# Kernel optimization log

Hardware: AMD Instinct MI355X
Metric: run time of the kernel (lower is better)

The kernel has to match this reference:

```python
import jax, jax.numpy as jnp
import numpy as np

N_NODES_PER_GRAPH = 64
NUM_GRAPHS = 2048
N = NUM_GRAPHS * N_NODES_PER_GRAPH  # 131072 total nodes
E = N * 8                           # 1048576 edges
IN_DIM, H1, H2 = 64, 128, 64
OUT_DIM = (N_NODES_PER_GRAPH * N_NODES_PER_GRAPH - N_NODES_PER_GRAPH) // 2  # 2016


def setup_inputs() -> dict:
    key = jax.random.key(0)
    ks = jax.random.split(key, 16)
    s = 0.05
    x = jax.random.normal(ks[0], (N, IN_DIM), dtype=jnp.float32)
    # edges within each graph: offsets within graph + graph base offset
    src_local = jax.random.randint(ks[1], (E,), 0, N_NODES_PER_GRAPH)
    dst_local = jax.random.randint(ks[2], (E,), 0, N_NODES_PER_GRAPH)
    gid = jnp.repeat(jnp.arange(NUM_GRAPHS), E // NUM_GRAPHS) * N_NODES_PER_GRAPH
    edge_index = jnp.stack([src_local + gid, dst_local + gid]).astype(jnp.int64)
    batch = jnp.repeat(jnp.arange(NUM_GRAPHS), N_NODES_PER_GRAPH).astype(jnp.int64)
    eps = jax.random.normal(ks[3], (NUM_GRAPHS, H2), dtype=jnp.float32)
    return {
        "x": x, "edge_index": edge_index, "batch": batch, "eps": eps,
        "w1_rel": jax.random.normal(ks[4], (IN_DIM, H1)) * s,
        "b1": jnp.zeros((H1,), jnp.float32),
        "w1_root": jax.random.normal(ks[5], (IN_DIM, H1)) * s,
        "w2_rel": jax.random.normal(ks[6], (H1, H2)) * s,
        "b2": jnp.zeros((H2,), jnp.float32),
        "w2_root": jax.random.normal(ks[7], (H1, H2)) * s,
        "w3_rel": jax.random.normal(ks[8], (H1, H2)) * s,
        "b3": jnp.zeros((H2,), jnp.float32),
        "w3_root": jax.random.normal(ks[9], (H1, H2)) * s,
        "fc1_w": jax.random.normal(ks[10], (H2, H1)) * s,
        "fc1_b": jnp.zeros((H1,), jnp.float32),
        "fc2_w": jax.random.normal(ks[11], (H1, OUT_DIM)) * s,
        "fc2_b": jnp.zeros((OUT_DIM,), jnp.float32),
    }


def _graph_conv(h, src, dst, w_rel, b, w_root):
    # PyG GraphConv: out_i = W_rel @ (sum_{j in N(i)} h_j) + b + W_root @ h_i
    agg = jax.ops.segment_sum(h[src], dst, num_segments=N)  # [N, d_in]
    return agg @ w_rel + b + h @ w_root


def _segment_mean(h, seg):
    s = jax.ops.segment_sum(h, seg, num_segments=NUM_GRAPHS)
    cnt = jax.ops.segment_sum(jnp.ones((h.shape[0],), h.dtype), seg, num_segments=NUM_GRAPHS)
    return s / jnp.maximum(cnt, 1.0)[:, None]


def reference(x, edge_index, batch, eps, w1_rel, b1, w1_root, w2_rel, b2, w2_root,
              w3_rel, b3, w3_root, fc1_w, fc1_b, fc2_w, fc2_b):
    src, dst = edge_index[0], edge_index[1]
    # encode (dropout p=0.0 -> identity)
    h1 = jax.nn.relu(_graph_conv(x, src, dst, w1_rel, b1, w1_root))
    mu = _segment_mean(_graph_conv(h1, src, dst, w2_rel, b2, w2_root), batch)
    logvar = _segment_mean(_graph_conv(h1, src, dst, w3_rel, b3, w3_root), batch)
    # reparameterize with provided eps
    z = mu + eps * jnp.exp(0.5 * logvar)
    # decode
    h = jax.nn.relu(z @ fc1_w + fc1_b)
    recon = jax.nn.sigmoid(h @ fc2_w + fc2_b)
    return recon, mu, logvar
```

## Files before the change

### kernel.cpp

```cpp
#include <hip/hip_runtime.h>
#include <math.h>

#define NG 2048
#define NPG 64
#define EPG 512
#define ETOT (NG*EPG)
#define IND 64
#define H1D 128
#define H2D 64
#define OUTD 2016

typedef __attribute__((ext_vector_type(8))) short bf16x8;
typedef __attribute__((ext_vector_type(4))) float f32x4;

__device__ inline short f2b(float f) {
  union { float f; unsigned u; } v; v.f = f;
  unsigned r = (v.u + 0x7FFFu + ((v.u >> 16) & 1u)) >> 16;
  return (short)r;
}

__global__ void p_w1(const float* __restrict__ w1_rel, const float* __restrict__ w1_root,
                     short* __restrict__ WTgF) {
  const int ct = blockIdx.x;
  const int ks = threadIdx.x >> 6, l = threadIdx.x & 63;
  const int col = ct*16 + (l & 15);
  const int kb  = ks*32 + (l >> 4)*8;
  short tmp[8];
  #pragma unroll
  for (int j = 0; j < 8; ++j) {
    const int k = kb + j;
    float v = (k < 64) ? w1_rel[k*H1D + col] : w1_root[(k - 64)*H1D + col];
    tmp[j] = f2b(v);
  }
  *(uint4*)&WTgF[(size_t)((ct*4 + ks)*64 + l)*8] = *(uint4*)tmp;
}

__global__ __launch_bounds__(256, 5) void k1_encoder(
    const float* __restrict__ x, const int* __restrict__ ei,
    const short* __restrict__ WTgF, const float* __restrict__ b1,
    float* __restrict__ SVp,
    const float* __restrict__ fc2_w, const float* __restrict__ w2_rel, const float* __restrict__ w2_root,
    const float* __restrict__ w3_rel, const float* __restrict__ w3_root,
    const float* __restrict__ fc1_w,
    short* __restrict__ WF2g, short* __restrict__ W23T, short* __restrict__ fc1T)
{
  __shared__ __align__(16) char smem[32768];
  const int g = blockIdx.x;
  const int tid = threadIdx.x;

  if (g >= NG) {
    float* L = (float*)smem;
    const int bid = g - NG;
    if (bid < 63) {
      const int c0 = bid*32;
      for (int i = tid; i < 4096; i += 256) {
        int k = i >> 5, c = i & 31;
        L[k*33 + c] = fc2_w[(size_t)k*OUTD + c0 + c];
      }
      __syncthreads();
      const int tl = tid >> 7;
      const int r  = tid & 127;
      const int ks = r >> 5;
      const int lp = r & 31;
      const int ct = bid*2 + tl;
      #pragma unroll
      for (int u = 0; u < 2; ++u) {
        const int l = lp*2 + u;
        const int cl = tl*16 + (l & 15);
        const int kb = ks*32 + (l >> 4)*8;
        short tmp[8];
        #pragma unroll
        for (int j = 0; j < 8; ++j) tmp[j] = f2b(L[(kb + j)*33 + cl]);
        *(uint4*)&WF2g[(size_t)((ct*4 + ks)*64 + l)*8] = *(uint4*)tmp;
      }
    } else if (bid < 67) {
      const int cc = bid - 63;
      const int j0 = cc*32;
      const float* wrel  = (cc < 2) ? w2_rel  : w3_rel;
      const float* wroot = (cc < 2) ? w2_root : w3_root;
      const int jl = j0 & 63;
      const int c = tid >> 3, k0 = (tid & 7)*32;
      for (int i = tid; i < 4096; i += 256) {
        int k = i >> 5, cc2 = i & 31;
        L[k*33 + cc2] = wrel[k*H2D + jl + cc2];
      }
      __syncthreads();
      if (k0 < 128)
        for (int kk = 0; kk < 32; ++kk)
          W23T[(size_t)(j0 + c)*264 + k0 + kk] = f2b(L[(k0 + kk)*33 + c]);
      __syncthreads();
      for (int i = tid; i < 4096; i += 256) {
        int k = i >> 5, cc2 = i & 31;
        L[k*33 + cc2] = wroot[k*H2D + jl + cc2];
      }
      __syncthreads();
      if (k0 >= 128)
        for (int kk = 0; kk < 32; ++kk)
          W23T[(size_t)(j0 + c)*264 + k0 + kk] = f2b(L[(k0 + kk - 128)*33 + c]);
    } else {
      const int c0 = (bid - 67)*64;
      for (int i = tid; i < 4096; i += 256) {
        int k = i >> 6, c = i & 63;
        L[k*65 + c] = fc1_w[k*H1D + c0 + c];
      }
      __syncthreads();
      const int c = tid >> 2, k0 = (tid & 3)*16;
      for (int kk = 0; kk < 16; ++kk)
        fc1T[(size_t)(c0 + c)*72 + k0 + kk] = f2b(L[(k0 + kk)*65 + c]);
    }
    return;
  }

  short* Xb   = (short*)smem;
  short* XbT  = (short*)(smem + 9216);
  short* Ab   = (short*)(smem + 18432);
  unsigned* Au32 = (unsigned*)(smem + 27648);

  const int w = tid >> 6, l = tid & 63;

  const int e0 = g*EPG + tid*2;
  const int s0 = ei[e0] & 63,     d0 = ei[ETOT + e0] & 63;
  const int s1 = ei[e0 + 1] & 63, d1 = ei[ETOT + e0 + 1] & 63;
  const int n = tid >> 2, f0 = (tid & 3) * 16;
  const float* xr = x + (size_t)g*(NPG*IND) + n*IND + f0;
  float4 v0 = *(const float4*)&xr[0];
  float4 v1 = *(const float4*)&xr[4];
  float4 v2 = *(const float4*)&xr[8];
  float4 v3 = *(const float4*)&xr[12];

  for (int i = tid; i < 64*16; i += 256) Au32[i] = 0u;
  __syncthreads();

  atomicAdd(&Au32[d0*16 + (s0 >> 2)], 1u << (8*(s0 & 3)));
  atomicAdd(&Au32[d1*16 + (s1 >> 2)], 1u << (8*(s1 & 3)));

  {
    short b[16];
    b[0]=f2b(v0.x); b[1]=f2b(v0.y); b[2]=f2b(v0.z); b[3]=f2b(v0.w);
    b[4]=f2b(v1.x); b[5]=f2b(v1.y); b[6]=f2b(v1.z); b[7]=f2b(v1.w);
    b[8]=f2b(v2.x); b[9]=f2b(v2.y); b[10]=f2b(v2.z); b[11]=f2b(v2.w);
    b[12]=f2b(v3.x); b[13]=f2b(v3.y); b[14]=f2b(v3.z); b[15]=f2b(v3.w);
    short* xbp = &Xb[n*72 + f0];
    #pragma unroll
    for (int j = 0; j < 16; ++j) xbp[j] = b[j];
    #pragma unroll
    for (int j = 0; j < 16; ++j) XbT[(f0 + j)*72 + n] = b[j];
  }
  __syncthreads();

  {
    const int row = tid >> 2, qw = tid & 3;
    unsigned wds[4];
    #pragma unroll
    for (int q = 0; q < 4; ++q) wds[q] = Au32[row*16 + qw*4 + q];
    unsigned* abp = (unsigned*)&Ab[row*72 + qw*16];
    #pragma unroll
    for (int q = 0; q < 4; ++q) {
      unsigned wv = wds[q];
      #pragma unroll
      for (int p = 0; p < 2; ++p) {
        unsigned c0 = (wv >> (16*p)) & 255u, c1 = (wv >> (16*p + 8)) & 255u;
        abp[q*2 + p] = (unsigned)(unsigned short)f2b((float)c0)
                     | ((unsigned)(unsigned short)f2b((float)c1) << 16);
      }
    }
  }

  float dg[4];
  {
    unsigned ps = 0;
    #pragma unroll
    for (int i = 0; i < 4; ++i) ps += Au32[((l >> 2) + 16*i)*16 + 4*w + (l & 3)];
    ps += __shfl_xor(ps, 4);
    ps += __shfl_xor(ps, 8);
    ps += __shfl_xor(ps, 16);
    ps += __shfl_xor(ps, 32);
    unsigned dword = __shfl(ps, (l >> 4));
    dg[0] = (float)(dword & 255u);
    dg[1] = (float)((dword >> 8) & 255u);
    dg[2] = (float)((dword >> 16) & 255u);
    dg[3] = (float)(dword >> 24);
  }

  const int rm = w*16;
  const int fr = l & 15;
  const int koff = (l >> 4) * 8;

  f32x4 agc[4];
  #pragma unroll
  for (int t = 0; t < 4; ++t) agc[t] = (f32x4){0.f,0.f,0.f,0.f};
  #pragma unroll
  for (int ks = 0; ks < 2; ++ks) {
    bf16x8 a = *(const bf16x8*)&Ab[(rm + fr)*72 + ks*32 + koff];
    #pragma unroll
    for (int t = 0; t < 4; ++t) {
      bf16x8 b = *(const bf16x8*)&XbT[(t*16 + fr)*72 + ks*32 + koff];
      agc[t] = __builtin_amdgcn_mfma_f32_16x16x32_bf16(a, b, agc[t], 0, 0, 0);
    }
  }
  short* AGb = Ab;
  #pragma unroll
  for (int t = 0; t < 4; ++t)
    #pragma unroll
    for (int r = 0; r < 4; ++r)
      AGb[(rm + (l>>4)*4 + r)*72 + t*16 + fr] = f2b(agc[t][r]);

  {
    bf16x8 afr[4];
    #pragma unroll
    for (int ks = 0; ks < 4; ++ks)
      afr[ks] = (ks < 2)
        ? *(const bf16x8*)&AGb[(rm + fr)*72 + ks*32 + koff]
        : *(const bf16x8*)&Xb[(rm + fr)*72 + (ks-2)*32 + koff];

    f32x4 acc[8];
    #pragma unroll
    for (int t = 0; t < 8; ++t) acc[t] = (f32x4){0.f,0.f,0.f,0.f};
    #pragma unroll
    for (int t = 0; t < 8; ++t)
      #pragma unroll
      for (int ks = 0; ks < 4; ++ks) {
        bf16x8 b = *(const bf16x8*)&WTgF[(size_t)((t*4 + ks)*64 + l)*8];
        acc[t] = __builtin_amdgcn_mfma_f32_16x16x32_bf16(afr[ks], b, acc[t], 0, 0, 0);
      }

    float* SVp_g = SVp + (size_t)(g*4 + w)*256;
    #pragma unroll
    for (int t = 0; t < 8; ++t) {
      const int col = t*16 + fr;
      const float bb = b1[col];
      float hs = 0.f, ws = 0.f;
      #pragma unroll
      for (int r = 0; r < 4; ++r) {
        float v = fmaxf(acc[t][r] + bb, 0.f);
        hs += v; ws += dg[r]*v;
      }
      hs += __shfl_down(hs, 32); ws += __shfl_down(ws, 32);
      hs += __shfl_down(hs, 16); ws += __shfl_down(ws, 16);
      if (l < 16) {
        SVp_g[col]       = ws;
        SVp_g[128 + col] = hs;
      }
    }
  }
}

__global__ __launch_bounds__(256) void k1b_latent(
    const float* __restrict__ SVp, const short* __restrict__ W23T,
    const float* __restrict__ b2, const float* __restrict__ b3,
    const float* __restrict__ eps, const short* __restrict__ fc1T,
    const float* __restrict__ fc1_b,
    float* __restrict__ out_mu, float* __restrict__ out_lv, short* __restrict__ hbufF)
{
  __shared__ short SV[32*264];
  __shared__ short Zt[32*72];
  const int g0 = blockIdx.x * 32;
  const int tid = threadIdx.x;
  const int w = tid >> 6, l = tid & 63;
  const int s = w >> 1;
  const int h = w & 1;
  const int fr = l & 15;
  const int koff = (l >> 4) * 8;

  for (int i = tid; i < 32*256; i += 256) {
    const int r = i >> 8, k = i & 255;
    const float* p4 = SVp + (size_t)(g0 + r)*1024 + k;
    float v = (p4[0] + p4[256]) + (p4[512] + p4[768]);
    SV[r*264 + k] = f2b(v);
  }
  __syncthreads();

  f32x4 acc[4];
  #pragma unroll
  for (int t = 0; t < 4; ++t) acc[t] = (f32x4){0.f,0.f,0.f,0.f};
  #pragma unroll
  for (int ks = 0; ks < 8; ++ks) {
    bf16x8 a = *(const bf16x8*)&SV[(s*16 + fr)*264 + ks*32 + koff];
    #pragma unroll
    for (int j = 0; j < 2; ++j) {
      bf16x8 bm = *(const bf16x8*)&W23T[((2*h + j)*16 + fr)*264 + ks*32 + koff];
      bf16x8 bl = *(const bf16x8*)&W23T[((2*h + j + 4)*16 + fr)*264 + ks*32 + koff];
      acc[j]     = __builtin_amdgcn_mfma_f32_16x16x32_bf16(a, bm, acc[j], 0, 0, 0);
      acc[2 + j] = __builtin_amdgcn_mfma_f32_16x16x32_bf16(a, bl, acc[2 + j], 0, 0, 0);
    }
  }
  #pragma unroll
  for (int j = 0; j < 2; ++j) {
    const int col = (2*h + j)*16 + fr;
    const float bb2 = b2[col], bb3 = b3[col];
    #pragma unroll
    for (int r = 0; r < 4; ++r) {
      const int row = s*16 + (l>>4)*4 + r;
      const size_t gg = (size_t)(g0 + row);
      float mu = acc[j][r]     * (1.f/64.f) + bb2;
      float lv = acc[2 + j][r] * (1.f/64.f) + bb3;
      out_mu[gg*64 + col] = mu;
      out_lv[gg*64 + col] = lv;
      float z = mu + eps[gg*64 + col] * __expf(0.5f*lv);
      Zt[row*72 + col] = f2b(z);
    }
  }
  __syncthreads();

  f32x4 hacc[4];
  #pragma unroll
  for (int t = 0; t < 4; ++t) hacc[t] = (f32x4){0.f,0.f,0.f,0.f};
  #pragma unroll
  for (int ks = 0; ks < 2; ++ks) {
    bf16x8 a = *(const bf16x8*)&Zt[(s*16 + fr)*72 + ks*32 + koff];
    #pragma unroll
    for (int j = 0; j < 4; ++j) {
      bf16x8 b = *(const bf16x8*)&fc1T[((h*4 + j)*16 + fr)*72 + ks*32 + koff];
      hacc[j] = __builtin_amdgcn_mfma_f32_16x16x32_bf16(a, b, hacc[j], 0, 0, 0);
    }
  }
  #pragma unroll
  for (int j = 0; j < 4; ++j) {
    const int col = (h*4 + j)*16 + fr;
    const int ks  = col >> 5;
    const int q   = (col >> 3) & 3;
    const int j8  = col & 7;
    const float bb = fc1_b[col];
    #pragma unroll
    for (int r = 0; r < 4; ++r) {
      const int row = s*16 + (l>>4)*4 + r;
      const int rt  = blockIdx.x*2 + (row >> 4);
      const int lane = (row & 15) + 16*q;
      hbufF[(size_t)((rt*4 + ks)*64 + lane)*8 + j8] = f2b(fmaxf(hacc[j][r] + bb, 0.f));
    }
  }
}

__global__ __launch_bounds__(256, 8) void k2_decoder(
    const short* __restrict__ hbufF, const short* __restrict__ WF2g,
    const float* __restrict__ fc2_b, float* __restrict__ recon)
{
  const int bx = blockIdx.x, by = blockIdx.y;
  const int tid = threadIdx.x;
  const int w = tid >> 6, l = tid & 63;
  const int fr = l & 15;
  const int rt = bx*4 + w;

  bf16x8 afr[4];
  #pragma unroll
  for (int ks = 0; ks < 4; ++ks)
    afr[ks] = *(const bf16x8*)&hbufF[(size_t)((rt*4 + ks)*64 + l)*8];

  f32x4 acc[6];
  #pragma unroll
  for (int t = 0; t < 6; ++t) acc[t] = (f32x4){0.f,0.f,0.f,0.f};

  #pragma unroll
  for (int ks = 0; ks < 4; ++ks) {
    #pragma unroll
    for (int t = 0; t < 6; ++t) {
      const int ct = by*6 + t;
      bf16x8 b = *(const bf16x8*)&WF2g[(size_t)((ct*4 + ks)*64 + l)*8];
      acc[t] = __builtin_amdgcn_mfma_f32_16x16x32_bf16(afr[ks], b, acc[t], 0, 0, 0);
    }
  }

  #pragma unroll
  for (int t = 0; t < 6; ++t) {
    const int col = by*96 + t*16 + fr;
    const float bb = fc2_b[col];
    #pragma unroll
    for (int r = 0; r < 4; ++r) {
      const int row = bx*64 + w*16 + (l>>4)*4 + r;
      float v = acc[t][r] + bb;
      recon[(size_t)row*OUTD + col] = 1.f/(1.f + __expf(-v));
    }
  }
}

extern "C" void kernel_launch(void* const* d_in, const int* in_sizes, int n_in,
                              void* d_out, int out_size, void* d_ws, size_t ws_size,
                              hipStream_t stream) {
  const float* x       = (const float*)d_in[0];
  const int*   ei      = (const int*)d_in[1];
  const float* eps     = (const float*)d_in[3];
  const float* w1_rel  = (const float*)d_in[4];
  const float* b1      = (const float*)d_in[5];
  const float* w1_root = (const float*)d_in[6];
  const float* w2_rel  = (const float*)d_in[7];
  const float* b2      = (const float*)d_in[8];
  const float* w2_root = (const float*)d_in[9];
  const float* w3_rel  = (const float*)d_in[10];
  const float* b3      = (const float*)d_in[11];
  const float* w3_root = (const float*)d_in[12];
  const float* fc1_w   = (const float*)d_in[13];
  const float* fc1_b   = (const float*)d_in[14];
  const float* fc2_w   = (const float*)d_in[15];
  const float* fc2_b   = (const float*)d_in[16];

  float* recon  = (float*)d_out;
  float* out_mu = recon + (size_t)NG*OUTD;
  float* out_lv = out_mu + (size_t)NG*H2D;

  char* p = (char*)d_ws;
  short* WTgF  = (short*)p;              p += 8*4*64*8*2;
  short* WF2g  = (short*)p;              p += 126*4*64*8*2;
  short* fc1T  = (short*)p;              p += 128*72*2;
  short* W23T  = (short*)p;              p += 128*264*2;
  float* SVp   = (float*)p;              p += (size_t)NG*4*256*4;
  short* hbufF = (short*)p;

  p_w1<<<8, 256, 0, stream>>>(w1_rel, w1_root, WTgF);
  k1_encoder<<<NG + 69, 256, 0, stream>>>(x, ei, WTgF, b1, SVp,
      fc2_w, w2_rel, w2_root, w3_rel, w3_root, fc1_w, WF2g, W23T, fc1T);
  k1b_latent<<<64, 256, 0, stream>>>(SVp, W23T, b2, b3, eps, fc1T, fc1_b,
                                     out_mu, out_lv, hbufF);
  k2_decoder<<<dim3(32, 21), 256, 0, stream>>>(hbufF, WF2g, fc2_b, recon);
}
```

Before: 144.2 us.

## Fuse latent stage into encoder via last-block atomic counter, restructure conv1 per-wave columns

Removes the separate latent kernel. The last of every 32 encoder blocks, detected with an atomic counter plus threadfence, now runs the mu/logvar/z/fc1 computation. Each wave now owns two output column tiles across all row tiles, so the per-graph sums reduce within the wave and SV is written once as bf16 instead of four fp32 partials. Weight prep for W2/W3/fc1 moves into the small prep kernel. Also vectorizes edge loads and LDS stores, and precomputes degrees into LDS. This trades one launch and the partial-sum traffic for a serialized tail in the last-arriving blocks and extra fences.

```diff
diff --git a/kernel.cpp b/kernel.cpp
--- a/kernel.cpp
+++ b/kernel.cpp
@@ -12,6 +12,8 @@
 
 typedef __attribute__((ext_vector_type(8))) short bf16x8;
 typedef __attribute__((ext_vector_type(4))) float f32x4;
+typedef __attribute__((ext_vector_type(8))) unsigned short u16x8;
+typedef __attribute__((ext_vector_type(4))) short s16x4;
 
 __device__ inline short f2b(float f) {
   union { float f; unsigned u; } v; v.f = f;
@@ -20,29 +22,76 @@
 }
 
 __global__ void p_w1(const float* __restrict__ w1_rel, const float* __restrict__ w1_root,
-                     short* __restrict__ WTgF) {
-  const int ct = blockIdx.x;
-  const int ks = threadIdx.x >> 6, l = threadIdx.x & 63;
-  const int col = ct*16 + (l & 15);
-  const int kb  = ks*32 + (l >> 4)*8;
-  short tmp[8];
-  #pragma unroll
-  for (int j = 0; j < 8; ++j) {
-    const int k = kb + j;
-    float v = (k < 64) ? w1_rel[k*H1D + col] : w1_root[(k - 64)*H1D + col];
-    tmp[j] = f2b(v);
-  }
-  *(uint4*)&WTgF[(size_t)((ct*4 + ks)*64 + l)*8] = *(uint4*)tmp;
+                     short* __restrict__ WTgF,
+                     const float* __restrict__ w2_rel, const float* __restrict__ w2_root,
+                     const float* __restrict__ w3_rel, const float* __restrict__ w3_root,
+                     const float* __restrict__ fc1_w,
+                     short* __restrict__ W23T, short* __restrict__ fc1T,
+                     unsigned* __restrict__ ctr) {
+  __shared__ float L[4224];
+  const int b = blockIdx.x;
+  const int tid = threadIdx.x;
+  if (b < 8) {
+    if (b == 0 && tid < 64) ctr[tid] = 0u;
+    const int ct = b;
+    const int ks = tid >> 6, l = tid & 63;
+    const int col = ct*16 + (l & 15);
+    const int kb  = ks*32 + (l >> 4)*8;
+    short tmp[8];
+    #pragma unroll
+    for (int j = 0; j < 8; ++j) {
+      const int k = kb + j;
+      float v = (k < 64) ? w1_rel[k*H1D + col] : w1_root[(k - 64)*H1D + col];
+      tmp[j] = f2b(v);
+    }
+    *(uint4*)&WTgF[(size_t)((ct*4 + ks)*64 + l)*8] = *(uint4*)tmp;
+  } else if (b < 12) {
+    const int cc = b - 8;
+    const int j0 = cc*32;
+    const float* wrel  = (cc < 2) ? w2_rel  : w3_rel;
+    const float* wroot = (cc < 2) ? w2_root : w3_root;
+    const int jl = j0 & 63;
+    const int c = tid >> 3, k0 = (tid & 7)*32;
+    for (int i = tid; i < 4096; i += 256) {
+      int k = i >> 5, cc2 = i & 31;
+      L[k*33 + cc2] = wrel[k*H2D + jl + cc2];
+    }
+    __syncthreads();
+    if (k0 < 128)
+      for (int kk = 0; kk < 32; ++kk)
+        W23T[(size_t)(j0 + c)*264 + k0 + kk] = f2b(L[(k0 + kk)*33 + c]);
+    __syncthreads();
+    for (int i = tid; i < 4096; i += 256) {
+      int k = i >> 5, cc2 = i & 31;
+      L[k*33 + cc2] = wroot[k*H2D + jl + cc2];
+    }
+    __syncthreads();
+    if (k0 >= 128)
+      for (int kk = 0; kk < 32; ++kk)
+        W23T[(size_t)(j0 + c)*264 + k0 + kk] = f2b(L[(k0 + kk - 128)*33 + c]);
+  } else {
+    const int c0 = (b - 12)*64;
+    for (int i = tid; i < 4096; i += 256) {
+      int k = i >> 6, c = i & 63;
+      L[k*65 + c] = fc1_w[k*H1D + c0 + c];
+    }
+    __syncthreads();
+    const int c = tid >> 2, k0 = (tid & 3)*16;
+    for (int kk = 0; kk < 16; ++kk)
+      fc1T[(size_t)(c0 + c)*72 + k0 + kk] = f2b(L[(k0 + kk)*65 + c]);
+  }
 }
 
-__global__ __launch_bounds__(256, 5) void k1_encoder(
+__global__ __launch_bounds__(256, 5) void k1_enc(
     const float* __restrict__ x, const int* __restrict__ ei,
     const short* __restrict__ WTgF, const float* __restrict__ b1,
-    float* __restrict__ SVp,
-    const float* __restrict__ fc2_w, const float* __restrict__ w2_rel, const float* __restrict__ w2_root,
-    const float* __restrict__ w3_rel, const float* __restrict__ w3_root,
-    const float* __restrict__ fc1_w,
-    short* __restrict__ WF2g, short* __restrict__ W23T, short* __restrict__ fc1T)
+    short* __restrict__ SVb,
+    const float* __restrict__ fc2_w, short* __restrict__ WF2g,
+    const short* __restrict__ W23T, const float* __restrict__ b2v,
+    const float* __restrict__ b3v, const float* __restrict__ eps,
+    const short* __restrict__ fc1T, const float* __restrict__ fc1_b,
+    float* __restrict__ out_mu, float* __restrict__ out_lv,
+    short* __restrict__ hbufF, unsigned* __restrict__ ctr)
 {
   __shared__ __align__(16) char smem[32768];
   const int g = blockIdx.x;
@@ -51,62 +100,26 @@
   if (g >= NG) {
     float* L = (float*)smem;
     const int bid = g - NG;
-    if (bid < 63) {
-      const int c0 = bid*32;
-      for (int i = tid; i < 4096; i += 256) {
-        int k = i >> 5, c = i & 31;
-        L[k*33 + c] = fc2_w[(size_t)k*OUTD + c0 + c];
-      }
-      __syncthreads();
-      const int tl = tid >> 7;
-      const int r  = tid & 127;
-      const int ks = r >> 5;
-      const int lp = r & 31;
-      const int ct = bid*2 + tl;
+    const int c0 = bid*32;
+    for (int i = tid; i < 4096; i += 256) {
+      int k = i >> 5, c = i & 31;
+      L[k*33 + c] = fc2_w[(size_t)k*OUTD + c0 + c];
+    }
+    __syncthreads();
+    const int tl = tid >> 7;
+    const int r  = tid & 127;
+    const int ks = r >> 5;
+    const int lp = r & 31;
+    const int ct = bid*2 + tl;
+    #pragma unroll
+    for (int u = 0; u < 2; ++u) {
+      const int l = lp*2 + u;
+      const int cl = tl*16 + (l & 15);
+      const int kb = ks*32 + (l >> 4)*8;
+      short tmp[8];
       #pragma unroll
-      for (int u = 0; u < 2; ++u) {
-        const int l = lp*2 + u;
-        const int cl = tl*16 + (l & 15);
-        const int kb = ks*32 + (l >> 4)*8;
-        short tmp[8];
-        #pragma unroll
-        for (int j = 0; j < 8; ++j) tmp[j] = f2b(L[(kb + j)*33 + cl]);
-        *(uint4*)&WF2g[(size_t)((ct*4 + ks)*64 + l)*8] = *(uint4*)tmp;
-      }
-    } else if (bid < 67) {
-      const int cc = bid - 63;
-      const int j0 = cc*32;
-      const float* wrel  = (cc < 2) ? w2_rel  : w3_rel;
-      const float* wroot = (cc < 2) ? w2_root : w3_root;
-      const int jl = j0 & 63;
-      const int c = tid >> 3, k0 = (tid & 7)*32;
-      for (int i = tid; i < 4096; i += 256) {
-        int k = i >> 5, cc2 = i & 31;
-        L[k*33 + cc2] = wrel[k*H2D + jl + cc2];
-      }
-      __syncthreads();
-      if (k0 < 128)
-        for (int kk = 0; kk < 32; ++kk)
-          W23T[(size_t)(j0 + c)*264 + k0 + kk] = f2b(L[(k0 + kk)*33 + c]);
-      __syncthreads();
-      for (int i = tid; i < 4096; i += 256) {
-        int k = i >> 5, cc2 = i & 31;
-        L[k*33 + cc2] = wroot[k*H2D + jl + cc2];
-      }
-      __syncthreads();
-      if (k0 >= 128)
-        for (int kk = 0; kk < 32; ++kk)
-          W23T[(size_t)(j0 + c)*264 + k0 + kk] = f2b(L[(k0 + kk - 128)*33 + c]);
-    } else {
-      const int c0 = (bid - 67)*64;
-      for (int i = tid; i < 4096; i += 256) {
-        int k = i >> 6, c = i & 63;
-        L[k*65 + c] = fc1_w[k*H1D + c0 + c];
-      }
-      __syncthreads();
-      const int c = tid >> 2, k0 = (tid & 3)*16;
-      for (int kk = 0; kk < 16; ++kk)
-        fc1T[(size_t)(c0 + c)*72 + k0 + kk] = f2b(L[(k0 + kk)*65 + c]);
+      for (int j = 0; j < 8; ++j) tmp[j] = f2b(L[(kb + j)*33 + cl]);
+      *(uint4*)&WF2g[(size_t)((ct*4 + ks)*64 + l)*8] = *(uint4*)tmp;
     }
     return;
   }
@@ -115,12 +128,15 @@
   short* XbT  = (short*)(smem + 9216);
   short* Ab   = (short*)(smem + 18432);
   unsigned* Au32 = (unsigned*)(smem + 27648);
+  float* Dg   = (float*)(smem + 31744);
 
   const int w = tid >> 6, l = tid & 63;
 
   const int e0 = g*EPG + tid*2;
-  const int s0 = ei[e0] & 63,     d0 = ei[ETOT + e0] & 63;
-  const int s1 = ei[e0 + 1] & 63, d1 = ei[ETOT + e0 + 1] & 63;
+  const int2 sp = *(const int2*)&ei[e0];
+  const int2 dp = *(const int2*)&ei[ETOT + e0];
+  const int s0 = sp.x & 63, d0 = dp.x & 63;
+  const int s1 = sp.y & 63, d1 = dp.y & 63;
   const int n = tid >> 2, f0 = (tid & 3) * 16;
   const float* xr = x + (size_t)g*(NPG*IND) + n*IND + f0;
   float4 v0 = *(const float4*)&xr[0];
@@ -135,16 +151,22 @@
   atomicAdd(&Au32[d1*16 + (s1 >> 2)], 1u << (8*(s1 & 3)));
 
   {
-    short b[16];
-    b[0]=f2b(v0.x); b[1]=f2b(v0.y); b[2]=f2b(v0.z); b[3]=f2b(v0.w);
-    b[4]=f2b(v1.x); b[5]=f2b(v1.y); b[6]=f2b(v1.z); b[7]=f2b(v1.w);
-    b[8]=f2b(v2.x); b[9]=f2b(v2.y); b[10]=f2b(v2.z); b[11]=f2b(v2.w);
-    b[12]=f2b(v3.x); b[13]=f2b(v3.y); b[14]=f2b(v3.z); b[15]=f2b(v3.w);
-    short* xbp = &Xb[n*72 + f0];
-    #pragma unroll
-    for (int j = 0; j < 16; ++j) xbp[j] = b[j];
-    #pragma unroll
-    for (int j = 0; j < 16; ++j) XbT[(f0 + j)*72 + n] = b[j];
+    u16x8 lo, hi;
+    lo[0]=(unsigned short)f2b(v0.x); lo[1]=(unsigned short)f2b(v0.y);
+    lo[2]=(unsigned short)f2b(v0.z); lo[3]=(unsigned short)f2b(v0.w);
+    lo[4]=(unsigned short)f2b(v1.x); lo[5]=(unsigned short)f2b(v1.y);
+    lo[6]=(unsigned short)f2b(v1.z); lo[7]=(unsigned short)f2b(v1.w);
+    hi[0]=(unsigned short)f2b(v2.x); hi[1]=(unsigned short)f2b(v2.y);
+    hi[2]=(unsigned short)f2b(v2.z); hi[3]=(unsigned short)f2b(v2.w);
+    hi[4]=(unsigned short)f2b(v3.x); hi[5]=(unsigned short)f2b(v3.y);
+    hi[6]=(unsigned short)f2b(v3.z); hi[7]=(unsigned short)f2b(v3.w);
+    *(u16x8*)&Xb[n*72 + f0]     = lo;
+    *(u16x8*)&Xb[n*72 + f0 + 8] = hi;
+    #pragma unroll
+    for (int j = 0; j < 8; ++j) {
+      XbT[(f0 + j)*72 + n]     = (short)lo[j];
+      XbT[(f0 + 8 + j)*72 + n] = (short)hi[j];
+    }
   }
   __syncthreads();
 
@@ -153,33 +175,31 @@
     unsigned wds[4];
     #pragma unroll
     for (int q = 0; q < 4; ++q) wds[q] = Au32[row*16 + qw*4 + q];
+    auto pk = [](unsigned wv, int p) -> unsigned {
+      unsigned c0 = (wv >> (16*p)) & 255u, c1 = (wv >> (16*p + 8)) & 255u;
+      return (unsigned)(unsigned short)f2b((float)c0)
+           | ((unsigned)(unsigned short)f2b((float)c1) << 16);
+    };
+    uint4 oA = { pk(wds[0],0), pk(wds[0],1), pk(wds[1],0), pk(wds[1],1) };
+    uint4 oB = { pk(wds[2],0), pk(wds[2],1), pk(wds[3],0), pk(wds[3],1) };
     unsigned* abp = (unsigned*)&Ab[row*72 + qw*16];
-    #pragma unroll
-    for (int q = 0; q < 4; ++q) {
-      unsigned wv = wds[q];
-      #pragma unroll
-      for (int p = 0; p < 2; ++p) {
-        unsigned c0 = (wv >> (16*p)) & 255u, c1 = (wv >> (16*p + 8)) & 255u;
-        abp[q*2 + p] = (unsigned)(unsigned short)f2b((float)c0)
-                     | ((unsigned)(unsigned short)f2b((float)c1) << 16);
-      }
-    }
-  }
-
-  float dg[4];
+    *(uint4*)&abp[0] = oA;
+    *(uint4*)&abp[4] = oB;
+  }
+
   {
+    const int squad = tid >> 4;
+    const int db = (tid & 15) * 4;
     unsigned ps = 0;
     #pragma unroll
-    for (int i = 0; i < 4; ++i) ps += Au32[((l >> 2) + 16*i)*16 + 4*w + (l & 3)];
-    ps += __shfl_xor(ps, 4);
-    ps += __shfl_xor(ps, 8);
-    ps += __shfl_xor(ps, 16);
-    ps += __shfl_xor(ps, 32);
-    unsigned dword = __shfl(ps, (l >> 4));
-    dg[0] = (float)(dword & 255u);
-    dg[1] = (float)((dword >> 8) & 255u);
-    dg[2] = (float)((dword >> 16) & 255u);
-    dg[3] = (float)(dword >> 24);
+    for (int i = 0; i < 4; ++i) ps += Au32[(db + i)*16 + squad];
+    ps += __shfl_xor(ps, 1); ps += __shfl_xor(ps, 2);
+    ps += __shfl_xor(ps, 4); ps += __shfl_xor(ps, 8);
+    if ((tid & 15) == 0) {
+      f32x4 dv = { (float)(ps & 255u), (float)((ps >> 8) & 255u),
+                   (float)((ps >> 16) & 255u), (float)(ps >> 24) };
+      *(f32x4*)&Dg[squad*4] = dv;
+    }
   }
 
   const int rm = w*16;
@@ -198,6 +218,14 @@
       agc[t] = __builtin_amdgcn_mfma_f32_16x16x32_bf16(a, b, agc[t], 0, 0, 0);
     }
   }
+
+  bf16x8 bfr[2][4];
+  #pragma unroll
+  for (int ct2 = 0; ct2 < 2; ++ct2)
+    #pragma unroll
+    for (int ks = 0; ks < 4; ++ks)
+      bfr[ct2][ks] = *(const bf16x8*)&WTgF[(size_t)(((2*w + ct2)*4 + ks)*64 + l)*8];
+
   short* AGb = Ab;
   #pragma unroll
   for (int t = 0; t < 4; ++t)
@@ -205,128 +233,124 @@
     for (int r = 0; r < 4; ++r)
       AGb[(rm + (l>>4)*4 + r)*72 + t*16 + fr] = f2b(agc[t][r]);
 
-  {
+  __syncthreads();
+
+  const float bb0 = b1[(2*w)*16 + fr];
+  const float bb1 = b1[(2*w + 1)*16 + fr];
+  float hs0 = 0.f, ws0 = 0.f, hs1 = 0.f, ws1 = 0.f;
+  #pragma unroll
+  for (int rt = 0; rt < 4; ++rt) {
     bf16x8 afr[4];
     #pragma unroll
     for (int ks = 0; ks < 4; ++ks)
       afr[ks] = (ks < 2)
-        ? *(const bf16x8*)&AGb[(rm + fr)*72 + ks*32 + koff]
-        : *(const bf16x8*)&Xb[(rm + fr)*72 + (ks-2)*32 + koff];
-
-    f32x4 acc[8];
-    #pragma unroll
-    for (int t = 0; t < 8; ++t) acc[t] = (f32x4){0.f,0.f,0.f,0.f};
-    #pragma unroll
-    for (int t = 0; t < 8; ++t)
+        ? *(const bf16x8*)&AGb[(rt*16 + fr)*72 + ks*32 + koff]
+        : *(const bf16x8*)&Xb[(rt*16 + fr)*72 + (ks - 2)*32 + koff];
+    f32x4 a0 = (f32x4){0.f,0.f,0.f,0.f}, a1 = (f32x4){0.f,0.f,0.f,0.f};
+    #pragma unroll
+    for (int ks = 0; ks < 4; ++ks) {
+      a0 = __builtin_amdgcn_mfma_f32_16x16x32_bf16(afr[ks], bfr[0][ks], a0, 0, 0, 0);
+      a1 = __builtin_amdgcn_mfma_f32_16x16x32_bf16(afr[ks], bfr[1][ks], a1, 0, 0, 0);
+    }
+    f32x4 dgv = *(const f32x4*)&Dg[rt*16 + (l >> 4)*4];
+    #pragma unroll
+    for (int r = 0; r < 4; ++r) {
+      float va = fmaxf(a0[r] + bb0, 0.f);
+      float vb = fmaxf(a1[r] + bb1, 0.f);
+      hs0 += va; ws0 += dgv[r]*va;
+      hs1 += vb; ws1 += dgv[r]*vb;
+    }
+  }
+  hs0 += __shfl_down(hs0, 32); ws0 += __shfl_down(ws0, 32);
+  hs1 += __shfl_down(hs1, 32); ws1 += __shfl_down(ws1, 32);
+  hs0 += __shfl_down(hs0, 16); ws0 += __shfl_down(ws0, 16);
+  hs1 += __shfl_down(hs1, 16); ws1 += __shfl_down(ws1, 16);
+  if (l < 16) {
+    short* svg = SVb + (size_t)g*256;
+    svg[(2*w)*16 + l]           = f2b(ws0);
+    svg[(2*w + 1)*16 + l]       = f2b(ws1);
+    svg[128 + (2*w)*16 + l]     = f2b(hs0);
+    svg[128 + (2*w + 1)*16 + l] = f2b(hs1);
+  }
+
+  __threadfence();
+  __syncthreads();
+  bool last = false;
+  if (tid == 0) last = (atomicAdd(&ctr[g >> 5], 1u) == 31u);
+  if (__syncthreads_count((int)last) == 0) return;
+  __threadfence();
+
+  {
+    const int g0 = g & ~31;
+    short* SVsh = (short*)smem;
+    short* Zt   = (short*)(smem + 16896);
+    const int s2 = w >> 1;
+    const int h  = w & 1;
+
+    for (int i = tid; i < 32*64; i += 256) {
+      const int r = i >> 6, kq = (i & 63)*4;
+      *(s16x4*)&SVsh[r*264 + kq] = *(const s16x4*)&SVb[(size_t)(g0 + r)*256 + kq];
+    }
+    __syncthreads();
+
+    f32x4 acc[4];
+    #pragma unroll
+    for (int t = 0; t < 4; ++t) acc[t] = (f32x4){0.f,0.f,0.f,0.f};
+    #pragma unroll
+    for (int ks = 0; ks < 8; ++ks) {
+      bf16x8 a = *(const bf16x8*)&SVsh[(s2*16 + fr)*264 + ks*32 + koff];
       #pragma unroll
-      for (int ks = 0; ks < 4; ++ks) {
-        bf16x8 b = *(const bf16x8*)&WTgF[(size_t)((t*4 + ks)*64 + l)*8];
-        acc[t] = __builtin_amdgcn_mfma_f32_16x16x32_bf16(afr[ks], b, acc[t], 0, 0, 0);
+      for (int j = 0; j < 2; ++j) {
+        bf16x8 bm = *(const bf16x8*)&W23T[((2*h + j)*16 + fr)*264 + ks*32 + koff];
+        bf16x8 bl = *(const bf16x8*)&W23T[((2*h + j + 4)*16 + fr)*264 + ks*32 + koff];
+        acc[j]     = __builtin_amdgcn_mfma_f32_16x16x32_bf16(a, bm, acc[j], 0, 0, 0);
+        acc[2 + j] = __builtin_amdgcn_mfma_f32_16x16x32_bf16(a, bl, acc[2 + j], 0, 0, 0);
       }
-
-    float* SVp_g = SVp + (size_t)(g*4 + w)*256;
-    #pragma unroll
-    for (int t = 0; t < 8; ++t) {
-      const int col = t*16 + fr;
-      const float bb = b1[col];
-      float hs = 0.f, ws = 0.f;
+    }
+    #pragma unroll
+    for (int j = 0; j < 2; ++j) {
+      const int col = (2*h + j)*16 + fr;
+      const float bb2 = b2v[col], bb3 = b3v[col];
       #pragma unroll
       for (int r = 0; r < 4; ++r) {
-        float v = fmaxf(acc[t][r] + bb, 0.f);
-        hs += v; ws += dg[r]*v;
+        const int row = s2*16 + (l>>4)*4 + r;
+        const size_t gg = (size_t)(g0 + row);
+        float mu = acc[j][r]     * (1.f/64.f) + bb2;
+        float lv = acc[2 + j][r] * (1.f/64.f) + bb3;
+        out_mu[gg*64 + col] = mu;
+        out_lv[gg*64 + col] = lv;
+        float z = mu + eps[gg*64 + col] * __expf(0.5f*lv);
+        Zt[row*72 + col] = f2b(z);
       }
-      hs += __shfl_down(hs, 32); ws += __shfl_down(ws, 32);
-      hs += __shfl_down(hs, 16); ws += __shfl_down(ws, 16);
-      if (l < 16) {
-        SVp_g[col]       = ws;
-        SVp_g[128 + col] = hs;
+    }
+    __syncthreads();
+
+    f32x4 hacc[4];
+    #pragma unroll
+    for (int t = 0; t < 4; ++t) hacc[t] = (f32x4){0.f,0.f,0.f,0.f};
+    #pragma unroll
+    for (int ks = 0; ks < 2; ++ks) {
+      bf16x8 a = *(const bf16x8*)&Zt[(s2*16 + fr)*72 + ks*32 + koff];
+      #pragma unroll
+      for (int j = 0; j < 4; ++j) {
+        bf16x8 b = *(const bf16x8*)&fc1T[((h*4 + j)*16 + fr)*72 + ks*32 + koff];
+        hacc[j] = __builtin_amdgcn_mfma_f32_16x16x32_bf16(a, b, hacc[j], 0, 0, 0);
       }
     }
-  }
-}
-
-__global__ __launch_bounds__(256) void k1b_latent(
-    const float* __restrict__ SVp, const short* __restrict__ W23T,
-    const float* __restrict__ b2, const float* __restrict__ b3,
-    const float* __restrict__ eps, const short* __restrict__ fc1T,
-    const float* __restrict__ fc1_b,
-    float* __restrict__ out_mu, float* __restrict__ out_lv, short* __restrict__ hbufF)
-{
-  __shared__ short SV[32*264];
-  __shared__ short Zt[32*72];
-  const int g0 = blockIdx.x * 32;
-  const int tid = threadIdx.x;
-  const int w = tid >> 6, l = tid & 63;
-  const int s = w >> 1;
-  const int h = w & 1;
-  const int fr = l & 15;
-  const int koff = (l >> 4) * 8;
-
-  for (int i = tid; i < 32*256; i += 256) {
-    const int r = i >> 8, k = i & 255;
-    const float* p4 = SVp + (size_t)(g0 + r)*1024 + k;
-    float v = (p4[0] + p4[256]) + (p4[512] + p4[768]);
-    SV[r*264 + k] = f2b(v);
-  }
-  __syncthreads();
-
-  f32x4 acc[4];
-  #pragma unroll
-  for (int t = 0; t < 4; ++t) acc[t] = (f32x4){0.f,0.f,0.f,0.f};
-  #pragma unroll
-  for (int ks = 0; ks < 8; ++ks) {
-    bf16x8 a = *(const bf16x8*)&SV[(s*16 + fr)*264 + ks*32 + koff];
-    #pragma unroll
-    for (int j = 0; j < 2; ++j) {
-      bf16x8 bm = *(const bf16x8*)&W23T[((2*h + j)*16 + fr)*264 + ks*32 + koff];
-      bf16x8 bl = *(const bf16x8*)&W23T[((2*h + j + 4)*16 + fr)*264 + ks*32 + koff];
-      acc[j]     = __builtin_amdgcn_mfma_f32_16x16x32_bf16(a, bm, acc[j], 0, 0, 0);
-      acc[2 + j] = __builtin_amdgcn_mfma_f32_16x16x32_bf16(a, bl, acc[2 + j], 0, 0, 0);
-    }
-  }
-  #pragma unroll
-  for (int j = 0; j < 2; ++j) {
-    const int col = (2*h + j)*16 + fr;
-    const float bb2 = b2[col], bb3 = b3[col];
-    #pragma unroll
-    for (int r = 0; r < 4; ++r) {
-      const int row = s*16 + (l>>4)*4 + r;
-      const size_t gg = (size_t)(g0 + row);
-      float mu = acc[j][r]     * (1.f/64.f) + bb2;
-      float lv = acc[2 + j][r] * (1.f/64.f) + bb3;
-      out_mu[gg*64 + col] = mu;
-      out_lv[gg*64 + col] = lv;
-      float z = mu + eps[gg*64 + col] * __expf(0.5f*lv);
-      Zt[row*72 + col] = f2b(z);
-    }
-  }
-  __syncthreads();
-
-  f32x4 hacc[4];
-  #pragma unroll
-  for (int t = 0; t < 4; ++t) hacc[t] = (f32x4){0.f,0.f,0.f,0.f};
-  #pragma unroll
-  for (int ks = 0; ks < 2; ++ks) {
-    bf16x8 a = *(const bf16x8*)&Zt[(s*16 + fr)*72 + ks*32 + koff];
     #pragma unroll
     for (int j = 0; j < 4; ++j) {
-      bf16x8 b = *(const bf16x8*)&fc1T[((h*4 + j)*16 + fr)*72 + ks*32 + koff];
-      hacc[j] = __builtin_amdgcn_mfma_f32_16x16x32_bf16(a, b, hacc[j], 0, 0, 0);
-    }
-  }
-  #pragma unroll
-  for (int j = 0; j < 4; ++j) {
-    const int col = (h*4 + j)*16 + fr;
-    const int ks  = col >> 5;
-    const int q   = (col >> 3) & 3;
-    const int j8  = col & 7;
-    const float bb = fc1_b[col];
-    #pragma unroll
-    for (int r = 0; r < 4; ++r) {
-      const int row = s*16 + (l>>4)*4 + r;
-      const int rt  = blockIdx.x*2 + (row >> 4);
-      const int lane = (row & 15) + 16*q;
-      hbufF[(size_t)((rt*4 + ks)*64 + lane)*8 + j8] = f2b(fmaxf(hacc[j][r] + bb, 0.f));
+      const int col = (h*4 + j)*16 + fr;
+      const int ks2 = col >> 5;
+      const int q   = (col >> 3) & 3;
+      const int j8  = col & 7;
+      const float bb = fc1_b[col];
+      #pragma unroll
+      for (int r = 0; r < 4; ++r) {
+        const int row = s2*16 + (l>>4)*4 + r;
+        const int rt2 = (g0 >> 4) + (row >> 4);
+        const int lane = (row & 15) + 16*q;
+        hbufF[(size_t)((rt2*4 + ks2)*64 + lane)*8 + j8] = f2b(fmaxf(hacc[j][r] + bb, 0.f));
+      }
     }
   }
 }
@@ -402,13 +426,14 @@
   short* WF2g  = (short*)p;              p += 126*4*64*8*2;
   short* fc1T  = (short*)p;              p += 128*72*2;
   short* W23T  = (short*)p;              p += 128*264*2;
-  float* SVp   = (float*)p;              p += (size_t)NG*4*256*4;
-  short* hbufF = (short*)p;
-
-  p_w1<<<8, 256, 0, stream>>>(w1_rel, w1_root, WTgF);
-  k1_encoder<<<NG + 69, 256, 0, stream>>>(x, ei, WTgF, b1, SVp,
-      fc2_w, w2_rel, w2_root, w3_rel, w3_root, fc1_w, WF2g, W23T, fc1T);
-  k1b_latent<<<64, 256, 0, stream>>>(SVp, W23T, b2, b3, eps, fc1T, fc1_b,
-                                     out_mu, out_lv, hbufF);
+  short* SVb   = (short*)p;              p += (size_t)NG*256*2;
+  short* hbufF = (short*)p;              p += (size_t)128*4*64*8*2;
+  unsigned* ctr = (unsigned*)p;
+
+  p_w1<<<14, 256, 0, stream>>>(w1_rel, w1_root, WTgF,
+                               w2_rel, w2_root, w3_rel, w3_root,
+                               fc1_w, W23T, fc1T, ctr);
+  k1_enc<<<NG + 63, 256, 0, stream>>>(x, ei, WTgF, b1, SVb,
+      fc2_w, WF2g, W23T, b2, b3, eps, fc1T, fc1_b, out_mu, out_lv, hbufF, ctr);
   k2_decoder<<<dim3(32, 21), 256, 0, stream>>>(hbufF, WF2g, fc2_b, recon);
 }
```

Result: slower. 324.2 us (+124.7%).
